# Kernel tuning notes

Hardware: AMD Instinct MI355X
Metric: run time of the kernel (lower is better)

Reference implementation:

```python
import jax, jax.numpy as jnp
import numpy as np

B, C, H, W = 4, 512, 64, 64
NUM_GROUPS = 32
EPS = 1e-6


def setup_inputs() -> dict:
    key = jax.random.key(0)
    ks = jax.random.split(key, 5)
    s = 1.0 / np.sqrt(C)
    return {
        "x": jax.random.normal(ks[0], (B, C, H, W), dtype=jnp.float32),
        "gn_scale": jnp.ones((C,), jnp.float32),
        "gn_bias": jnp.zeros((C,), jnp.float32),
        "wq": jax.random.normal(ks[1], (C, C), jnp.float32) * s,
        "bq": jnp.zeros((C,), jnp.float32),
        "wk": jax.random.normal(ks[2], (C, C), jnp.float32) * s,
        "bk": jnp.zeros((C,), jnp.float32),
        "wv": jax.random.normal(ks[3], (C, C), jnp.float32) * s,
        "bv": jnp.zeros((C,), jnp.float32),
        "wo": jax.random.normal(ks[4], (C, C), jnp.float32) * s,
        "bo": jnp.zeros((C,), jnp.float32),
    }


def _group_norm(x, scale, bias):
    # x: [b, c, h, w]; normalize over (c//g, h, w) within each of g groups
    b, c, h, w = x.shape
    g = NUM_GROUPS
    xg = x.reshape(b, g, c // g, h, w)
    mean = jnp.mean(xg, axis=(2, 3, 4), keepdims=True)
    var = jnp.var(xg, axis=(2, 3, 4), keepdims=True)
    xg = (xg - mean) * jax.lax.rsqrt(var + EPS)
    xn = xg.reshape(b, c, h, w)
    return xn * scale[None, :, None, None] + bias[None, :, None, None]


def _conv1x1(x, w, b):
    # channel-mixing 1x1 conv: [b, c, h, w] x [c_in, c_out] -> [b, c_out, h, w]
    return jnp.einsum('bchw,cd->bdhw', x, w) + b[None, :, None, None]


def reference(x, gn_scale, gn_bias, wq, bq, wk, bk, wv, bv, wo, bo):
    b, c, h, w = x.shape
    h_ = _group_norm(x, gn_scale, gn_bias)
    q = _conv1x1(h_, wq, bq).reshape(b, c, h * w).transpose(0, 2, 1)  # [b, hw, c]
    k = _conv1x1(h_, wk, bk).reshape(b, c, h * w)                     # [b, c, hw]
    v = _conv1x1(h_, wv, bv).reshape(b, c, h * w)                     # [b, c, hw]
    scores = jnp.matmul(q, k) * (c ** -0.5)      # [b, hw, hw]
    attn = jax.nn.softmax(scores, axis=-1)       # [b, hw, hw]
    out = jnp.matmul(v, attn.transpose(0, 2, 1)) # [b, c, hw]
    out = out.reshape(b, c, h, w)
    out = _conv1x1(out, wo, bo)
    return x + out
```

## Files before the change

### kernel.cpp

```cpp
#include <hip/hip_runtime.h>
#include <stdint.h>

typedef __attribute__((ext_vector_type(8))) short short8;
typedef __attribute__((ext_vector_type(4))) float f32x4;
typedef __attribute__((ext_vector_type(16))) float f32x16;
typedef __attribute__((ext_vector_type(4))) unsigned int uint4v;

__device__ __forceinline__ short cvt_bf16(float f) {
  uint32_t u = __builtin_bit_cast(uint32_t, f);
  u += 0x7FFFu + ((u >> 16) & 1u);
  return (short)(u >> 16);
}

__device__ __forceinline__ float bf16_to_f32(short s) {
  return __builtin_bit_cast(float, (uint32_t)((unsigned short)s) << 16);
}

__device__ __forceinline__ void gload_lds16(const void* g, void* l) {
  __builtin_amdgcn_global_load_lds(
      (const __attribute__((address_space(1))) void*)g,
      (__attribute__((address_space(3))) void*)l, 16, 0, 0);
}

__global__ __launch_bounds__(256) void k_transpose_w(const float* __restrict__ src,
                                                     short* __restrict__ dst) {
  __shared__ float t[32][33];
  int n0 = blockIdx.x * 32, c0 = blockIdx.y * 32;
  int lx = threadIdx.x & 31, ly = threadIdx.x >> 5;
#pragma unroll
  for (int i = 0; i < 4; ++i) {
    int c = ly + i * 8;
    t[c][lx] = src[(size_t)(c0 + c) * 512 + n0 + lx];
  }
  __syncthreads();
#pragma unroll
  for (int i = 0; i < 4; ++i) {
    int n = ly + i * 8;
    dst[(size_t)(n0 + n) * 512 + c0 + lx] = cvt_bf16(t[lx][n]);
  }
}

__global__ void k_bias_concat(const float* __restrict__ bq, const float* __restrict__ bk,
                              float* __restrict__ bqk) {
  int i = blockIdx.x * 256 + threadIdx.x;
  if (i < 512) bqk[i] = bq[i];
  else if (i < 1024) bqk[i] = bk[i - 512];
}

__global__ __launch_bounds__(256) void k_gn_stats(const float* __restrict__ x,
                                                  float* __restrict__ stats) {
  int bg = blockIdx.x;
  const float* p = x + (size_t)bg * 65536;
  float s = 0.f, ss = 0.f;
#pragma unroll 4
  for (int i = 0; i < 64; ++i) {
    float4 v = *(const float4*)(p + i * 1024 + threadIdx.x * 4);
    s += v.x + v.y + v.z + v.w;
    ss += v.x * v.x + v.y * v.y + v.z * v.z + v.w * v.w;
  }
#pragma unroll
  for (int m = 1; m < 64; m <<= 1) {
    s += __shfl_xor(s, m, 64);
    ss += __shfl_xor(ss, m, 64);
  }
  __shared__ float red[8];
  int w = threadIdx.x >> 6;
  if ((threadIdx.x & 63) == 0) { red[w * 2] = s; red[w * 2 + 1] = ss; }
  __syncthreads();
  if (threadIdx.x == 0) {
    float S1 = red[0] + red[2] + red[4] + red[6];
    float S2 = red[1] + red[3] + red[5] + red[7];
    float mean = S1 * (1.f / 65536.f);
    float var = S2 * (1.f / 65536.f) - mean * mean;
    stats[bg * 2] = mean;
    stats[bg * 2 + 1] = rsqrtf(var + 1e-6f);
  }
}

__global__ __launch_bounds__(256) void k_gn_apply(const float* __restrict__ x,
    const float* __restrict__ stats, const float* __restrict__ gsc,
    const float* __restrict__ gbi, short* __restrict__ h_t) {
  __shared__ float t[64][65];
  int p0 = blockIdx.x * 64, c0 = blockIdx.y * 64, b = blockIdx.z;
  int lp = threadIdx.x & 63, lc = threadIdx.x >> 6;
#pragma unroll
  for (int i = 0; i < 16; ++i) {
    int c = c0 + lc * 16 + i;
    float mean = stats[(b * 32 + (c >> 4)) * 2];
    float rstd = stats[(b * 32 + (c >> 4)) * 2 + 1];
    float v = x[((size_t)b * 512 + c) * 4096 + p0 + lp];
    t[lc * 16 + i][lp] = (v - mean) * rstd * gsc[c] + gbi[c];
  }
  __syncthreads();
  int pl = threadIdx.x >> 2;
  int cs = (threadIdx.x & 3) * 16;
  short8 v8a, v8b;
#pragma unroll
  for (int j = 0; j < 8; ++j) v8a[j] = cvt_bf16(t[cs + j][pl]);
#pragma unroll
  for (int j = 0; j < 8; ++j) v8b[j] = cvt_bf16(t[cs + 8 + j][pl]);
  size_t o = ((size_t)(b * 4096 + p0 + pl)) * 512 + c0 + cs;
  *(short8*)(h_t + o) = v8a;
  *(short8*)(h_t + o + 8) = v8b;
}

template <int BIAS_M, int FINAL>
__global__ __launch_bounds__(256) void k_gemm(const short* __restrict__ A,
    const short* __restrict__ Bm, const float* __restrict__ bias,
    short* __restrict__ Cb, float* __restrict__ Cf, const float* __restrict__ resid,
    int ldc) {
  __shared__ __align__(16) short a_lds[128 * 32];
  __shared__ __align__(16) short b_lds[128 * 32];
  int m0 = blockIdx.x * 128, n0 = blockIdx.y * 128;
  int lane = threadIdx.x & 63, wid = threadIdx.x >> 6;
  int h16 = lane >> 4, l16 = lane & 15;
  int wr = wid >> 1, wc = wid & 1;

  f32x4 acc[4][4];
#pragma unroll
  for (int mi = 0; mi < 4; ++mi)
#pragma unroll
    for (int ni = 0; ni < 4; ++ni) acc[mi][ni] = (f32x4){0.f, 0.f, 0.f, 0.f};

  for (int kk = 0; kk < 16; ++kk) {
#pragma unroll
    for (int i = 0; i < 4; ++i) {
      int idx = wid * 4 + i;
      int mat = idx >> 3, h = (idx >> 1) & 3, rh = idx & 1;
      const short* src = (mat ? Bm : A) +
          ((size_t)((mat ? n0 : m0) + rh * 64 + lane)) * 512 + kk * 32 + h * 8;
      short* dst = (mat ? b_lds : a_lds) + (h * 128 + rh * 64) * 8;
      gload_lds16(src, dst);
    }
    asm volatile("s_waitcnt vmcnt(0)" ::: "memory");
    __syncthreads();
    short8 af[4], bf[4];
#pragma unroll
    for (int mi = 0; mi < 4; ++mi)
      af[mi] = *(const short8*)(a_lds + (h16 * 128 + wr * 64 + mi * 16 + l16) * 8);
#pragma unroll
    for (int ni = 0; ni < 4; ++ni)
      bf[ni] = *(const short8*)(b_lds + (h16 * 128 + wc * 64 + ni * 16 + l16) * 8);
#pragma unroll
    for (int mi = 0; mi < 4; ++mi)
#pragma unroll
      for (int ni = 0; ni < 4; ++ni)
        acc[mi][ni] = __builtin_amdgcn_mfma_f32_16x16x32_bf16(af[mi], bf[ni], acc[mi][ni], 0, 0, 0);
    __syncthreads();
  }

#pragma unroll
  for (int mi = 0; mi < 4; ++mi)
#pragma unroll
    for (int ni = 0; ni < 4; ++ni)
#pragma unroll
      for (int r = 0; r < 4; ++r) {
        int row = m0 + wr * 64 + mi * 16 + 4 * h16 + r;
        int col = n0 + wc * 64 + ni * 16 + l16;
        float v = acc[mi][ni][r] + (BIAS_M ? bias[row] : bias[col]);
        if (FINAL) {
          size_t oidx = ((size_t)((col >> 12) * 512 + row)) * 4096 + (col & 4095);
          Cf[oidx] = v + resid[oidx];
        } else {
          Cb[(size_t)row * ldc + col] = cvt_bf16(v);
        }
      }
}

__global__ __launch_bounds__(512, 2) void k_flash6(const short* __restrict__ qk,
    const short* __restrict__ v_t, short* __restrict__ oa, short* __restrict__ ob,
    float* __restrict__ ml) {
  __shared__ __align__(16) short k_lds[2 * 32 * 512];
  __shared__ __align__(16) short v_lds[32 * 512];
  __shared__ __align__(16) float s_lds[8 * 1024];

  const int tid = threadIdx.x;
  const int lane = tid & 63, wid = tid >> 6;
  const int qg = wid >> 1, dh = wid & 1;
  const int l31 = lane & 31, h = lane >> 5;
  const int bx = blockIdx.x;
  const int combo = bx & 7, qt = bx >> 3;
  const int b = combo >> 1, s = combo & 1;
  const float K2 = 0.06376649f;

  short8 qf[16];
  {
    const short* qbase = qk + ((size_t)(b * 4096 + qt * 128 + qg * 32 + l31)) * 1024
                         + dh * 256 + h * 8;
#pragma unroll
    for (int s_ = 0; s_ < 16; ++s_) qf[s_] = *(const short8*)(qbase + s_ * 16);
  }

  const size_t kvrow0 = (size_t)(b * 4096 + s * 2048);

#define STAGE_K6(T, DST)                                                              \
  {                                                                                   \
    int t_ = (T);                                                                     \
    short* d_ = (DST);                                                                \
    _Pragma("unroll") for (int i = 0; i < 4; ++i) {                                   \
      int ks = wid * 4 + i;                                                           \
      gload_lds16(qk + (kvrow0 + t_ * 32 + l31) * 1024 + 512 + ks * 16 + h * 8,       \
                  d_ + ks * 512);                                                     \
    }                                                                                 \
  }
#define STAGE_V6(T)                                                                   \
  {                                                                                   \
    int t_ = (T);                                                                     \
    _Pragma("unroll") for (int i = 0; i < 4; ++i) {                                   \
      int si = wid * 4 + i;                                                           \
      int ks = si >> 4, d0 = si & 15;                                                 \
      gload_lds16(v_t + (size_t)(d0 * 32 + l31) * 16384                               \
                      + (kvrow0 + t_ * 32 + ks * 16 + h * 8),                         \
                  v_lds + si * 512);                                                  \
    }                                                                                 \
  }

  STAGE_K6(0, k_lds);
  STAGE_V6(0);
  asm volatile("s_waitcnt vmcnt(0)" ::: "memory");
  __builtin_amdgcn_s_barrier();
  __builtin_amdgcn_sched_barrier(0);

  float m_run = -3.0e38f, l_run = 0.f;
  f32x16 acc[8];
#pragma unroll
  for (int tl = 0; tl < 8; ++tl)
#pragma unroll
    for (int r = 0; r < 16; ++r) acc[tl][r] = 0.f;

  for (int t = 0; t < 64; ++t) {
    const int kb = t & 1;
    const short* kcur = k_lds + kb * (32 * 512);
    short* knxt = k_lds + (kb ^ 1) * (32 * 512);
    if (t + 1 < 64) STAGE_K6(t + 1, knxt);
    f32x16 st;
#pragma unroll
    for (int r = 0; r < 16; ++r) st[r] = 0.f;
    __builtin_amdgcn_s_setprio(1);
#pragma unroll
    for (int s_ = 0; s_ < 16; ++s_) {
      short8 kf = *(const short8*)(kcur + ((dh * 16 + s_) * 64 + lane) * 8);
      st = __builtin_amdgcn_mfma_f32_32x32x16_bf16(kf, qf[s_], st, 0, 0, 0);
    }
    __builtin_amdgcn_s_setprio(0);
    {
      float* sp = s_lds + wid * 1024 + lane * 4;
#pragma unroll
      for (int q4 = 0; q4 < 4; ++q4) {
        f32x4 v = {st[q4 * 4 + 0], st[q4 * 4 + 1], st[q4 * 4 + 2], st[q4 * 4 + 3]};
        *(f32x4*)(sp + q4 * 256) = v;
      }
    }
    asm volatile("s_waitcnt vmcnt(4) lgkmcnt(0)" ::: "memory");
    __builtin_amdgcn_s_barrier();
    __builtin_amdgcn_sched_barrier(0);
    {
      const float* sp = s_lds + (wid ^ 1) * 1024 + lane * 4;
#pragma unroll
      for (int q4 = 0; q4 < 4; ++q4) {
        f32x4 v = *(const f32x4*)(sp + q4 * 256);
        st[q4 * 4 + 0] += v[0]; st[q4 * 4 + 1] += v[1];
        st[q4 * 4 + 2] += v[2]; st[q4 * 4 + 3] += v[3];
      }
    }
    float u0 = fmaxf(st[0], st[1]),  u1 = fmaxf(st[2], st[3]);
    float u2 = fmaxf(st[4], st[5]),  u3 = fmaxf(st[6], st[7]);
    float u4 = fmaxf(st[8], st[9]),  u5 = fmaxf(st[10], st[11]);
    float u6 = fmaxf(st[12], st[13]), u7 = fmaxf(st[14], st[15]);
    float mt = fmaxf(fmaxf(fmaxf(u0, u1), fmaxf(u2, u3)),
                     fmaxf(fmaxf(u4, u5), fmaxf(u6, u7)));
    mt = fmaxf(mt, __shfl_xor(mt, 32));
    if (__any(mt > m_run + 45.0f)) {
      float mnew = fmaxf(m_run, mt);
      float rs = exp2f((m_run - mnew) * K2);
      m_run = mnew;
      l_run *= rs;
#pragma unroll
      for (int r = 0; r < 16; ++r) {
        int rowq = (r & 3) + 8 * (r >> 2) + 4 * h;
        float rr = __shfl(rs, rowq);
#pragma unroll
        for (int tl = 0; tl < 8; ++tl) acc[tl][r] *= rr;
      }
    }
    float ls = 0.f;
#pragma unroll
    for (int r = 0; r < 16; ++r) { st[r] = exp2f((st[r] - m_run) * K2); ls += st[r]; }
    ls += __shfl_xor(ls, 32);
    l_run += ls;
    __builtin_amdgcn_s_setprio(1);
#pragma unroll
    for (int ks = 0; ks < 2; ++ks) {
      unsigned int a0, a1, a2, a3;
      int bse = ks * 8;
      asm("v_cvt_pk_bf16_f32 %0, %1, %2" : "=v"(a0) : "v"(st[bse + 0]), "v"(st[bse + 1]));
      asm("v_cvt_pk_bf16_f32 %0, %1, %2" : "=v"(a1) : "v"(st[bse + 2]), "v"(st[bse + 3]));
      asm("v_cvt_pk_bf16_f32 %0, %1, %2" : "=v"(a2) : "v"(st[bse + 4]), "v"(st[bse + 5]));
      asm("v_cvt_pk_bf16_f32 %0, %1, %2" : "=v"(a3) : "v"(st[bse + 6]), "v"(st[bse + 7]));
      asm("v_permlane32_swap_b32 %0, %1" : "+v"(a0), "+v"(a2));
      asm("v_permlane32_swap_b32 %0, %1" : "+v"(a1), "+v"(a3));
      uint4v w; w[0] = a0; w[1] = a1; w[2] = a2; w[3] = a3;
      short8 pa = __builtin_bit_cast(short8, w);
#pragma unroll
      for (int tl = 0; tl < 8; ++tl) {
        short8 vb = *(const short8*)(v_lds + ((ks * 16 + dh * 8 + tl) * 64 + lane) * 8);
        acc[tl] = __builtin_amdgcn_mfma_f32_32x32x16_bf16(pa, vb, acc[tl], 0, 0, 0);
      }
    }
    __builtin_amdgcn_s_setprio(0);
    asm volatile("s_waitcnt vmcnt(0) lgkmcnt(0)" ::: "memory");
    __builtin_amdgcn_s_barrier();
    __builtin_amdgcn_sched_barrier(0);
    if (t + 1 < 64) STAGE_V6(t + 1);
  }

  float linv = 1.0f / l_run;
  short* obuf = (s == 0) ? oa : ob;
#pragma unroll
  for (int r = 0; r < 16; ++r) {
    int rowq = (r & 3) + 8 * (r >> 2) + 4 * h;
    float li = __shfl(linv, rowq);
    size_t grow = ((size_t)(b * 4096 + qt * 128 + qg * 32 + rowq)) * 512;
#pragma unroll
    for (int tl = 0; tl < 8; ++tl)
      obuf[grow + dh * 256 + tl * 32 + l31] = cvt_bf16(acc[tl][r] * li);
  }
  if (dh == 0 && lane < 32) {
    int gq = b * 4096 + qt * 128 + qg * 32 + lane;
    ml[((size_t)s * 16384 + gq) * 2 + 0] = m_run;
    ml[((size_t)s * 16384 + gq) * 2 + 1] = l_run;
  }
#undef STAGE_K6
#undef STAGE_V6
}

__global__ __launch_bounds__(256) void k_combine(const short* __restrict__ oa,
    const float* __restrict__ ml, short* __restrict__ ob_out) {
  int gq = blockIdx.x * 4 + (threadIdx.x >> 6);
  int d0 = (threadIdx.x & 63) * 8;
  const float K2 = 0.06376649f;
  float ma = ml[(size_t)gq * 2 + 0], la = ml[(size_t)gq * 2 + 1];
  float mb = ml[((size_t)16384 + gq) * 2 + 0], lb = ml[((size_t)16384 + gq) * 2 + 1];
  float m = fmaxf(ma, mb);
  float wa = exp2f((ma - m) * K2) * la;
  float wb = exp2f((mb - m) * K2) * lb;
  float denom = wa + wb;
  float fa, fb;
  if (isfinite(denom) && denom > 0.f) {
    float inv = 1.f / denom;
    fa = wa * inv; fb = wb * inv;
  } else {
    fa = (ma >= mb) ? 1.f : 0.f;
    fb = 1.f - fa;
  }
  short8 a = *(const short8*)(oa + (size_t)gq * 512 + d0);
  short8 bv = *(const short8*)(ob_out + (size_t)gq * 512 + d0);
  short8 o;
#pragma unroll
  for (int j = 0; j < 8; ++j)
    o[j] = cvt_bf16(fa * bf16_to_f32(a[j]) + fb * bf16_to_f32(bv[j]));
  *(short8*)(ob_out + (size_t)gq * 512 + d0) = o;
}

extern "C" void kernel_launch(void* const* d_in, const int* in_sizes, int n_in,
                              void* d_out, int out_size, void* d_ws, size_t ws_size,
                              hipStream_t stream) {
  const float* x   = (const float*)d_in[0];
  const float* gsc = (const float*)d_in[1];
  const float* gbi = (const float*)d_in[2];
  const float* wq  = (const float*)d_in[3];
  const float* bq  = (const float*)d_in[4];
  const float* wk  = (const float*)d_in[5];
  const float* bk  = (const float*)d_in[6];
  const float* wv  = (const float*)d_in[7];
  const float* bv  = (const float*)d_in[8];
  const float* wo  = (const float*)d_in[9];
  const float* bo  = (const float*)d_in[10];
  float* out = (float*)d_out;

  char* ws = (char*)d_ws;
  float* stats = (float*)ws;
  float* bqk   = (float*)(ws + 4096);
  short* wqk_t = (short*)(ws + 16384);
  short* wv_t  = (short*)(ws + 16384 + (1u << 20));
  short* wo_t  = (short*)(ws + 16384 + (1u << 20) + (1u << 19));
  char*  big   = ws + 16384 + (1u << 21);
  short* h_t   = (short*)big;
  short* qkb   = (short*)(big + (16ll << 20));
  short* v_t   = (short*)(big + (48ll << 20));
  short* o_at  = (short*)(big + (64ll << 20));
  float* mlbuf = (float*)(big + (80ll << 20));

  dim3 b256(256);
  k_transpose_w<<<dim3(16, 16), b256, 0, stream>>>(wq, wqk_t);
  k_transpose_w<<<dim3(16, 16), b256, 0, stream>>>(wk, wqk_t + 512 * 512);
  k_transpose_w<<<dim3(16, 16), b256, 0, stream>>>(wv, wv_t);
  k_transpose_w<<<dim3(16, 16), b256, 0, stream>>>(wo, wo_t);
  k_bias_concat<<<4, 256, 0, stream>>>(bq, bk, bqk);
  k_gn_stats<<<128, b256, 0, stream>>>(x, stats);
  k_gn_apply<<<dim3(64, 8, 4), b256, 0, stream>>>(x, stats, gsc, gbi, h_t);
  k_gemm<0, 0><<<dim3(128, 8), b256, 0, stream>>>(h_t, wqk_t, bqk, qkb, nullptr, nullptr, 1024);
  k_gemm<1, 0><<<dim3(4, 128), b256, 0, stream>>>(wv_t, h_t, bv, v_t, nullptr, nullptr, 16384);
  k_flash6<<<dim3(256), dim3(512), 0, stream>>>(qkb, v_t, h_t, o_at, mlbuf);
  k_combine<<<dim3(4096), b256, 0, stream>>>(h_t, mlbuf, o_at);
  k_gemm<1, 1><<<dim3(4, 128), b256, 0, stream>>>(wo_t, o_at, bo, nullptr, out, x, 0);
}
```

Measured before the change: 401.7 us.

## Shrink flash attention blocks to 64 queries, single-buffer K, split QK accumulator chains

```diff
diff --git a/kernel.cpp b/kernel.cpp
--- a/kernel.cpp
+++ b/kernel.cpp
@@ -167,12 +167,12 @@
       }
 }
 
-__global__ __launch_bounds__(512, 2) void k_flash6(const short* __restrict__ qk,
+__global__ __launch_bounds__(256, 2) void k_flash7(const short* __restrict__ qk,
     const short* __restrict__ v_t, short* __restrict__ oa, short* __restrict__ ob,
     float* __restrict__ ml) {
-  __shared__ __align__(16) short k_lds[2 * 32 * 512];
+  __shared__ __align__(16) short k_lds[32 * 512];
   __shared__ __align__(16) short v_lds[32 * 512];
-  __shared__ __align__(16) float s_lds[8 * 1024];
+  __shared__ __align__(16) float s_lds[4 * 1024];
 
   const int tid = threadIdx.x;
   const int lane = tid & 63, wid = tid >> 6;
@@ -185,7 +185,7 @@
 
   short8 qf[16];
   {
-    const short* qbase = qk + ((size_t)(b * 4096 + qt * 128 + qg * 32 + l31)) * 1024
+    const short* qbase = qk + ((size_t)(b * 4096 + qt * 64 + qg * 32 + l31)) * 1024
                          + dh * 256 + h * 8;
 #pragma unroll
     for (int s_ = 0; s_ < 16; ++s_) qf[s_] = *(const short8*)(qbase + s_ * 16);
@@ -193,21 +193,20 @@
 
   const size_t kvrow0 = (size_t)(b * 4096 + s * 2048);
 
-#define STAGE_K6(T, DST)                                                              \
+#define STAGE_K7(T)                                                                   \
   {                                                                                   \
     int t_ = (T);                                                                     \
-    short* d_ = (DST);                                                                \
-    _Pragma("unroll") for (int i = 0; i < 4; ++i) {                                   \
-      int ks = wid * 4 + i;                                                           \
+    _Pragma("unroll") for (int i = 0; i < 8; ++i) {                                   \
+      int ks = wid * 8 + i;                                                           \
       gload_lds16(qk + (kvrow0 + t_ * 32 + l31) * 1024 + 512 + ks * 16 + h * 8,       \
-                  d_ + ks * 512);                                                     \
+                  k_lds + ks * 512);                                                  \
     }                                                                                 \
   }
-#define STAGE_V6(T)                                                                   \
+#define STAGE_V7(T)                                                                   \
   {                                                                                   \
     int t_ = (T);                                                                     \
-    _Pragma("unroll") for (int i = 0; i < 4; ++i) {                                   \
-      int si = wid * 4 + i;                                                           \
+    _Pragma("unroll") for (int i = 0; i < 8; ++i) {                                   \
+      int si = wid * 8 + i;                                                           \
       int ks = si >> 4, d0 = si & 15;                                                 \
       gload_lds16(v_t + (size_t)(d0 * 32 + l31) * 16384                               \
                       + (kvrow0 + t_ * 32 + ks * 16 + h * 8),                         \
@@ -215,8 +214,8 @@
     }                                                                                 \
   }
 
-  STAGE_K6(0, k_lds);
-  STAGE_V6(0);
+  STAGE_K7(0);
+  STAGE_V7(0);
   asm volatile("s_waitcnt vmcnt(0)" ::: "memory");
   __builtin_amdgcn_s_barrier();
   __builtin_amdgcn_sched_barrier(0);
@@ -229,20 +228,22 @@
     for (int r = 0; r < 16; ++r) acc[tl][r] = 0.f;
 
   for (int t = 0; t < 64; ++t) {
-    const int kb = t & 1;
-    const short* kcur = k_lds + kb * (32 * 512);
-    short* knxt = k_lds + (kb ^ 1) * (32 * 512);
-    if (t + 1 < 64) STAGE_K6(t + 1, knxt);
+    const int tn = (t + 1 < 64) ? t + 1 : 63;
+    f32x16 stA, stB;
+#pragma unroll
+    for (int r = 0; r < 16; ++r) { stA[r] = 0.f; stB[r] = 0.f; }
+    __builtin_amdgcn_s_setprio(1);
+#pragma unroll
+    for (int s_ = 0; s_ < 8; ++s_) {
+      short8 kfA = *(const short8*)(k_lds + ((dh * 16 + s_) * 64 + lane) * 8);
+      short8 kfB = *(const short8*)(k_lds + ((dh * 16 + 8 + s_) * 64 + lane) * 8);
+      stA = __builtin_amdgcn_mfma_f32_32x32x16_bf16(kfA, qf[s_], stA, 0, 0, 0);
+      stB = __builtin_amdgcn_mfma_f32_32x32x16_bf16(kfB, qf[8 + s_], stB, 0, 0, 0);
+    }
+    __builtin_amdgcn_s_setprio(0);
     f32x16 st;
 #pragma unroll
-    for (int r = 0; r < 16; ++r) st[r] = 0.f;
-    __builtin_amdgcn_s_setprio(1);
-#pragma unroll
-    for (int s_ = 0; s_ < 16; ++s_) {
-      short8 kf = *(const short8*)(kcur + ((dh * 16 + s_) * 64 + lane) * 8);
-      st = __builtin_amdgcn_mfma_f32_32x32x16_bf16(kf, qf[s_], st, 0, 0, 0);
-    }
-    __builtin_amdgcn_s_setprio(0);
+    for (int r = 0; r < 16; ++r) st[r] = stA[r] + stB[r];
     {
       float* sp = s_lds + wid * 1024 + lane * 4;
 #pragma unroll
@@ -251,9 +252,10 @@
         *(f32x4*)(sp + q4 * 256) = v;
       }
     }
-    asm volatile("s_waitcnt vmcnt(4) lgkmcnt(0)" ::: "memory");
+    asm volatile("s_waitcnt vmcnt(0) lgkmcnt(0)" ::: "memory");
     __builtin_amdgcn_s_barrier();
     __builtin_amdgcn_sched_barrier(0);
+    STAGE_K7(tn);
     {
       const float* sp = s_lds + (wid ^ 1) * 1024 + lane * 4;
 #pragma unroll
@@ -311,7 +313,7 @@
     asm volatile("s_waitcnt vmcnt(0) lgkmcnt(0)" ::: "memory");
     __builtin_amdgcn_s_barrier();
     __builtin_amdgcn_sched_barrier(0);
-    if (t + 1 < 64) STAGE_V6(t + 1);
+    STAGE_V7(tn);
   }
 
   float linv = 1.0f / l_run;
@@ -320,18 +322,18 @@
   for (int r = 0; r < 16; ++r) {
     int rowq = (r & 3) + 8 * (r >> 2) + 4 * h;
     float li = __shfl(linv, rowq);
-    size_t grow = ((size_t)(b * 4096 + qt * 128 + qg * 32 + rowq)) * 512;
+    size_t grow = ((size_t)(b * 4096 + qt * 64 + qg * 32 + rowq)) * 512;
 #pragma unroll
     for (int tl = 0; tl < 8; ++tl)
       obuf[grow + dh * 256 + tl * 32 + l31] = cvt_bf16(acc[tl][r] * li);
   }
   if (dh == 0 && lane < 32) {
-    int gq = b * 4096 + qt * 128 + qg * 32 + lane;
+    int gq = b * 4096 + qt * 64 + qg * 32 + lane;
     ml[((size_t)s * 16384 + gq) * 2 + 0] = m_run;
     ml[((size_t)s * 16384 + gq) * 2 + 1] = l_run;
   }
-#undef STAGE_K6
-#undef STAGE_V6
+#undef STAGE_K7
+#undef STAGE_V7
 }
 
 __global__ __launch_bounds__(256) void k_combine(const short* __restrict__ oa,
@@ -401,7 +403,7 @@
   k_gn_apply<<<dim3(64, 8, 4), b256, 0, stream>>>(x, stats, gsc, gbi, h_t);
   k_gemm<0, 0><<<dim3(128, 8), b256, 0, stream>>>(h_t, wqk_t, bqk, qkb, nullptr, nullptr, 1024);
   k_gemm<1, 0><<<dim3(4, 128), b256, 0, stream>>>(wv_t, h_t, bv, v_t, nullptr, nullptr, 16384);
-  k_flash6<<<dim3(256), dim3(512), 0, stream>>>(qkb, v_t, h_t, o_at, mlbuf);
+  k_flash7<<<dim3(512), b256, 0, stream>>>(qkb, v_t, h_t, o_at, mlbuf);
   k_combine<<<dim3(4096), b256, 0, stream>>>(h_t, mlbuf, o_at);
   k_gemm<1, 1><<<dim3(4, 128), b256, 0, stream>>>(wo_t, o_at, bo, nullptr, out, x, 0);
 }
```

New measurement: 548.8 us. +36.6%, slower.

## Software-pipeline flash attention: overlap QK of next tile with softmax/PV of previous

Applied to the files above, without the earlier changes.

```diff
diff --git a/kernel.cpp b/kernel.cpp
--- a/kernel.cpp
+++ b/kernel.cpp
@@ -167,11 +167,11 @@
       }
 }
 
-__global__ __launch_bounds__(512, 2) void k_flash6(const short* __restrict__ qk,
+__global__ __launch_bounds__(512, 2) void k_flash8(const short* __restrict__ qk,
     const short* __restrict__ v_t, short* __restrict__ oa, short* __restrict__ ob,
     float* __restrict__ ml) {
-  __shared__ __align__(16) short k_lds[2 * 32 * 512];
-  __shared__ __align__(16) short v_lds[32 * 512];
+  __shared__ __align__(16) short k_lds[32 * 512];
+  __shared__ __align__(16) short v_lds[2 * 32 * 512];
   __shared__ __align__(16) float s_lds[8 * 1024];
 
   const int tid = threadIdx.x;
@@ -193,125 +193,159 @@
 
   const size_t kvrow0 = (size_t)(b * 4096 + s * 2048);
 
-#define STAGE_K6(T, DST)                                                              \
+#define STAGE_K8(T)                                                                   \
+  {                                                                                   \
+    int t_ = (T);                                                                     \
+    _Pragma("unroll") for (int i = 0; i < 4; ++i) {                                   \
+      int ks = wid * 4 + i;                                                           \
+      gload_lds16(qk + (kvrow0 + t_ * 32 + l31) * 1024 + 512 + ks * 16 + h * 8,       \
+                  k_lds + ks * 512);                                                  \
+    }                                                                                 \
+  }
+#define STAGE_V8(T, DST)                                                              \
   {                                                                                   \
     int t_ = (T);                                                                     \
     short* d_ = (DST);                                                                \
-    _Pragma("unroll") for (int i = 0; i < 4; ++i) {                                   \
-      int ks = wid * 4 + i;                                                           \
-      gload_lds16(qk + (kvrow0 + t_ * 32 + l31) * 1024 + 512 + ks * 16 + h * 8,       \
-                  d_ + ks * 512);                                                     \
-    }                                                                                 \
-  }
-#define STAGE_V6(T)                                                                   \
-  {                                                                                   \
-    int t_ = (T);                                                                     \
     _Pragma("unroll") for (int i = 0; i < 4; ++i) {                                   \
       int si = wid * 4 + i;                                                           \
       int ks = si >> 4, d0 = si & 15;                                                 \
       gload_lds16(v_t + (size_t)(d0 * 32 + l31) * 16384                               \
                       + (kvrow0 + t_ * 32 + ks * 16 + h * 8),                         \
-                  v_lds + si * 512);                                                  \
-    }                                                                                 \
-  }
-
-  STAGE_K6(0, k_lds);
-  STAGE_V6(0);
+                  d_ + si * 512);                                                     \
+    }                                                                                 \
+  }
+#define QK8(ST)                                                                       \
+  _Pragma("unroll") for (int s_ = 0; s_ < 16; ++s_) {                                 \
+    short8 kf = *(const short8*)(k_lds + ((dh * 16 + s_) * 64 + lane) * 8);           \
+    ST = __builtin_amdgcn_mfma_f32_32x32x16_bf16(kf, qf[s_], ST, 0, 0, 0);            \
+  }
+#define SOFTMAX8(STC, PA)                                                             \
+  {                                                                                   \
+    float u0 = fmaxf(STC[0], STC[1]),  u1 = fmaxf(STC[2], STC[3]);                    \
+    float u2 = fmaxf(STC[4], STC[5]),  u3 = fmaxf(STC[6], STC[7]);                    \
+    float u4 = fmaxf(STC[8], STC[9]),  u5 = fmaxf(STC[10], STC[11]);                  \
+    float u6 = fmaxf(STC[12], STC[13]), u7 = fmaxf(STC[14], STC[15]);                 \
+    float mt = fmaxf(fmaxf(fmaxf(u0, u1), fmaxf(u2, u3)),                             \
+                     fmaxf(fmaxf(u4, u5), fmaxf(u6, u7)));                            \
+    mt = fmaxf(mt, __shfl_xor(mt, 32));                                               \
+    if (__any(mt > m_run + 45.0f)) {                                                  \
+      float mnew = fmaxf(m_run, mt);                                                  \
+      float rs = exp2f((m_run - mnew) * K2);                                          \
+      m_run = mnew;                                                                   \
+      l_run *= rs;                                                                    \
+      _Pragma("unroll") for (int r = 0; r < 16; ++r) {                                \
+        int rowq = (r & 3) + 8 * (r >> 2) + 4 * h;                                    \
+        float rr = __shfl(rs, rowq);                                                  \
+        _Pragma("unroll") for (int tl = 0; tl < 8; ++tl) acc[tl][r] *= rr;            \
+      }                                                                               \
+    }                                                                                 \
+    float ls = 0.f;                                                                   \
+    _Pragma("unroll") for (int r = 0; r < 16; ++r) {                                  \
+      STC[r] = exp2f((STC[r] - m_run) * K2); ls += STC[r];                            \
+    }                                                                                 \
+    ls += __shfl_xor(ls, 32);                                                         \
+    l_run += ls;                                                                      \
+    _Pragma("unroll") for (int ks = 0; ks < 2; ++ks) {                                \
+      unsigned int a0, a1, a2, a3;                                                    \
+      int bse = ks * 8;                                                               \
+      asm("v_cvt_pk_bf16_f32 %0, %1, %2" : "=v"(a0) : "v"(STC[bse+0]), "v"(STC[bse+1])); \
+      asm("v_cvt_pk_bf16_f32 %0, %1, %2" : "=v"(a1) : "v"(STC[bse+2]), "v"(STC[bse+3])); \
+      asm("v_cvt_pk_bf16_f32 %0, %1, %2" : "=v"(a2) : "v"(STC[bse+4]), "v"(STC[bse+5])); \
+      asm("v_cvt_pk_bf16_f32 %0, %1, %2" : "=v"(a3) : "v"(STC[bse+6]), "v"(STC[bse+7])); \
+      asm("v_permlane32_swap_b32 %0, %1" : "+v"(a0), "+v"(a2));                       \
+      asm("v_permlane32_swap_b32 %0, %1" : "+v"(a1), "+v"(a3));                       \
+      uint4v w; w[0] = a0; w[1] = a1; w[2] = a2; w[3] = a3;                           \
+      PA[ks] = __builtin_bit_cast(short8, w);                                         \
+    }                                                                                 \
+  }
+#define SWRITE8(ST)                                                                   \
+  {                                                                                   \
+    float* sp = s_lds + wid * 1024 + lane * 4;                                        \
+    _Pragma("unroll") for (int q4 = 0; q4 < 4; ++q4) {                                \
+      f32x4 v = {ST[q4*4+0], ST[q4*4+1], ST[q4*4+2], ST[q4*4+3]};                     \
+      *(f32x4*)(sp + q4 * 256) = v;                                                   \
+    }                                                                                 \
+  }
+#define SCOMBINE8(ST, STC)                                                            \
+  {                                                                                   \
+    const float* sp = s_lds + (wid ^ 1) * 1024 + lane * 4;                            \
+    _Pragma("unroll") for (int q4 = 0; q4 < 4; ++q4) {                                \
+      f32x4 v = *(const f32x4*)(sp + q4 * 256);                                       \
+      STC[q4*4+0] = ST[q4*4+0] + v[0]; STC[q4*4+1] = ST[q4*4+1] + v[1];               \
+      STC[q4*4+2] = ST[q4*4+2] + v[2]; STC[q4*4+3] = ST[q4*4+3] + v[3];               \
+    }                                                                                 \
+  }
+#define PV8(PA, VSRC)                                                                 \
+  _Pragma("unroll") for (int ks = 0; ks < 2; ++ks)                                    \
+    _Pragma("unroll") for (int tl = 0; tl < 8; ++tl) {                                \
+      short8 vb = *(const short8*)((VSRC) + ((ks * 16 + dh * 8 + tl) * 64 + lane) * 8); \
+      acc[tl] = __builtin_amdgcn_mfma_f32_32x32x16_bf16(PA[ks], vb, acc[tl], 0, 0, 0); \
+    }
+
+  float m_run = -3.0e38f, l_run = 0.f;
+  f32x16 acc[8];
+#pragma unroll
+  for (int tl = 0; tl < 8; ++tl)
+#pragma unroll
+    for (int r = 0; r < 16; ++r) acc[tl][r] = 0.f;
+
+  STAGE_K8(0);
+  STAGE_V8(0, v_lds);
   asm volatile("s_waitcnt vmcnt(0)" ::: "memory");
   __builtin_amdgcn_s_barrier();
   __builtin_amdgcn_sched_barrier(0);
 
-  float m_run = -3.0e38f, l_run = 0.f;
-  f32x16 acc[8];
-#pragma unroll
-  for (int tl = 0; tl < 8; ++tl)
-#pragma unroll
-    for (int r = 0; r < 16; ++r) acc[tl][r] = 0.f;
-
-  for (int t = 0; t < 64; ++t) {
-    const int kb = t & 1;
-    const short* kcur = k_lds + kb * (32 * 512);
-    short* knxt = k_lds + (kb ^ 1) * (32 * 512);
-    if (t + 1 < 64) STAGE_K6(t + 1, knxt);
+  f32x16 stC;
+  {
     f32x16 st;
 #pragma unroll
     for (int r = 0; r < 16; ++r) st[r] = 0.f;
     __builtin_amdgcn_s_setprio(1);
-#pragma unroll
-    for (int s_ = 0; s_ < 16; ++s_) {
-      short8 kf = *(const short8*)(kcur + ((dh * 16 + s_) * 64 + lane) * 8);
-      st = __builtin_amdgcn_mfma_f32_32x32x16_bf16(kf, qf[s_], st, 0, 0, 0);
-    }
+    QK8(st);
     __builtin_amdgcn_s_setprio(0);
-    {
-      float* sp = s_lds + wid * 1024 + lane * 4;
-#pragma unroll
-      for (int q4 = 0; q4 < 4; ++q4) {
-        f32x4 v = {st[q4 * 4 + 0], st[q4 * 4 + 1], st[q4 * 4 + 2], st[q4 * 4 + 3]};
-        *(f32x4*)(sp + q4 * 256) = v;
-      }
-    }
-    asm volatile("s_waitcnt vmcnt(4) lgkmcnt(0)" ::: "memory");
+    SWRITE8(st);
+    asm volatile("s_waitcnt lgkmcnt(0)" ::: "memory");
     __builtin_amdgcn_s_barrier();
     __builtin_amdgcn_sched_barrier(0);
-    {
-      const float* sp = s_lds + (wid ^ 1) * 1024 + lane * 4;
-#pragma unroll
-      for (int q4 = 0; q4 < 4; ++q4) {
-        f32x4 v = *(const f32x4*)(sp + q4 * 256);
-        st[q4 * 4 + 0] += v[0]; st[q4 * 4 + 1] += v[1];
-        st[q4 * 4 + 2] += v[2]; st[q4 * 4 + 3] += v[3];
-      }
-    }
-    float u0 = fmaxf(st[0], st[1]),  u1 = fmaxf(st[2], st[3]);
-    float u2 = fmaxf(st[4], st[5]),  u3 = fmaxf(st[6], st[7]);
-    float u4 = fmaxf(st[8], st[9]),  u5 = fmaxf(st[10], st[11]);
-    float u6 = fmaxf(st[12], st[13]), u7 = fmaxf(st[14], st[15]);
-    float mt = fmaxf(fmaxf(fmaxf(u0, u1), fmaxf(u2, u3)),
-                     fmaxf(fmaxf(u4, u5), fmaxf(u6, u7)));
-    mt = fmaxf(mt, __shfl_xor(mt, 32));
-    if (__any(mt > m_run + 45.0f)) {
-      float mnew = fmaxf(m_run, mt);
-      float rs = exp2f((m_run - mnew) * K2);
-      m_run = mnew;
-      l_run *= rs;
-#pragma unroll
-      for (int r = 0; r < 16; ++r) {
-        int rowq = (r & 3) + 8 * (r >> 2) + 4 * h;
-        float rr = __shfl(rs, rowq);
-#pragma unroll
-        for (int tl = 0; tl < 8; ++tl) acc[tl][r] *= rr;
-      }
-    }
-    float ls = 0.f;
-#pragma unroll
-    for (int r = 0; r < 16; ++r) { st[r] = exp2f((st[r] - m_run) * K2); ls += st[r]; }
-    ls += __shfl_xor(ls, 32);
-    l_run += ls;
+    STAGE_K8(1);
+    SCOMBINE8(st, stC);
+    asm volatile("s_waitcnt vmcnt(0) lgkmcnt(0)" ::: "memory");
+    __builtin_amdgcn_s_barrier();
+    __builtin_amdgcn_sched_barrier(0);
+    STAGE_V8(1, v_lds + 32 * 512);
+  }
+
+  for (int t = 1; t < 64; ++t) {
+    const int tn = (t + 1 < 64) ? t + 1 : 63;
+    const short* vprev = v_lds + ((t - 1) & 1) * (32 * 512);
+    short* vnext = v_lds + ((t + 1) & 1) * (32 * 512);
+    f32x16 st;
+#pragma unroll
+    for (int r = 0; r < 16; ++r) st[r] = 0.f;
     __builtin_amdgcn_s_setprio(1);
-#pragma unroll
-    for (int ks = 0; ks < 2; ++ks) {
-      unsigned int a0, a1, a2, a3;
-      int bse = ks * 8;
-      asm("v_cvt_pk_bf16_f32 %0, %1, %2" : "=v"(a0) : "v"(st[bse + 0]), "v"(st[bse + 1]));
-      asm("v_cvt_pk_bf16_f32 %0, %1, %2" : "=v"(a1) : "v"(st[bse + 2]), "v"(st[bse + 3]));
-      asm("v_cvt_pk_bf16_f32 %0, %1, %2" : "=v"(a2) : "v"(st[bse + 4]), "v"(st[bse + 5]));
-      asm("v_cvt_pk_bf16_f32 %0, %1, %2" : "=v"(a3) : "v"(st[bse + 6]), "v"(st[bse + 7]));
-      asm("v_permlane32_swap_b32 %0, %1" : "+v"(a0), "+v"(a2));
-      asm("v_permlane32_swap_b32 %0, %1" : "+v"(a1), "+v"(a3));
-      uint4v w; w[0] = a0; w[1] = a1; w[2] = a2; w[3] = a3;
-      short8 pa = __builtin_bit_cast(short8, w);
-#pragma unroll
-      for (int tl = 0; tl < 8; ++tl) {
-        short8 vb = *(const short8*)(v_lds + ((ks * 16 + dh * 8 + tl) * 64 + lane) * 8);
-        acc[tl] = __builtin_amdgcn_mfma_f32_32x32x16_bf16(pa, vb, acc[tl], 0, 0, 0);
-      }
-    }
+    QK8(st);
+    __builtin_amdgcn_s_setprio(0);
+    short8 pa[2];
+    SOFTMAX8(stC, pa);
+    SWRITE8(st);
+    asm volatile("s_waitcnt lgkmcnt(0)" ::: "memory");
+    __builtin_amdgcn_s_barrier();
+    __builtin_amdgcn_sched_barrier(0);
+    if (t < 63) STAGE_K8(tn);
+    SCOMBINE8(st, stC);
+    __builtin_amdgcn_s_setprio(1);
+    PV8(pa, vprev);
     __builtin_amdgcn_s_setprio(0);
     asm volatile("s_waitcnt vmcnt(0) lgkmcnt(0)" ::: "memory");
     __builtin_amdgcn_s_barrier();
     __builtin_amdgcn_sched_barrier(0);
-    if (t + 1 < 64) STAGE_V6(t + 1);
+    if (t < 63) STAGE_V8(tn, vnext);
+  }
+
+  {
+    short8 pa[2];
+    SOFTMAX8(stC, pa);
+    PV8(pa, v_lds + (63 & 1) * (32 * 512));
   }
 
   float linv = 1.0f / l_run;
@@ -330,8 +364,13 @@
     ml[((size_t)s * 16384 + gq) * 2 + 0] = m_run;
     ml[((size_t)s * 16384 + gq) * 2 + 1] = l_run;
   }
-#undef STAGE_K6
-#undef STAGE_V6
+#undef STAGE_K8
+#undef STAGE_V8
+#undef QK8
+#undef SOFTMAX8
+#undef SWRITE8
+#undef SCOMBINE8
+#undef PV8
 }
 
 __global__ __launch_bounds__(256) void k_combine(const short* __restrict__ oa,
@@ -401,7 +440,7 @@
   k_gn_apply<<<dim3(64, 8, 4), b256, 0, stream>>>(x, stats, gsc, gbi, h_t);
   k_gemm<0, 0><<<dim3(128, 8), b256, 0, stream>>>(h_t, wqk_t, bqk, qkb, nullptr, nullptr, 1024);
   k_gemm<1, 0><<<dim3(4, 128), b256, 0, stream>>>(wv_t, h_t, bv, v_t, nullptr, nullptr, 16384);
-  k_flash6<<<dim3(256), dim3(512), 0, stream>>>(qkb, v_t, h_t, o_at, mlbuf);
+  k_flash8<<<dim3(256), dim3(512), 0, stream>>>(qkb, v_t, h_t, o_at, mlbuf);
   k_combine<<<dim3(4096), b256, 0, stream>>>(h_t, mlbuf, o_at);
   k_gemm<1, 1><<<dim3(4, 128), b256, 0, stream>>>(wo_t, o_at, bo, nullptr, out, x, 0);
 }
```

After: 379.2 us. 5.6% less time.

## Process 64-key tiles per flash iteration with bf16 partial-score exchange

Applied to the files above, without the earlier changes.

```diff
diff --git a/kernel.cpp b/kernel.cpp
--- a/kernel.cpp
+++ b/kernel.cpp
@@ -14,6 +14,13 @@
 
 __device__ __forceinline__ float bf16_to_f32(short s) {
   return __builtin_bit_cast(float, (uint32_t)((unsigned short)s) << 16);
+}
+
+__device__ __forceinline__ float bflo(uint32_t u) {
+  return __builtin_bit_cast(float, u << 16);
+}
+__device__ __forceinline__ float bfhi(uint32_t u) {
+  return __builtin_bit_cast(float, u & 0xffff0000u);
 }
 
 __device__ __forceinline__ void gload_lds16(const void* g, void* l) {
@@ -167,12 +174,12 @@
       }
 }
 
-__global__ __launch_bounds__(512, 2) void k_flash6(const short* __restrict__ qk,
+__global__ __launch_bounds__(512, 2) void k_flash9(const short* __restrict__ qk,
     const short* __restrict__ v_t, short* __restrict__ oa, short* __restrict__ ob,
     float* __restrict__ ml) {
-  __shared__ __align__(16) short k_lds[2 * 32 * 512];
-  __shared__ __align__(16) short v_lds[32 * 512];
-  __shared__ __align__(16) float s_lds[8 * 1024];
+  __shared__ __align__(16) short k_lds[64 * 512];
+  __shared__ __align__(16) short v_lds[64 * 512];
+  __shared__ __align__(16) char  s_x[8 * 4096];
 
   const int tid = threadIdx.x;
   const int lane = tid & 63, wid = tid >> 6;
@@ -193,30 +200,31 @@
 
   const size_t kvrow0 = (size_t)(b * 4096 + s * 2048);
 
-#define STAGE_K6(T, DST)                                                              \
+#define STAGE_K9(T)                                                                   \
   {                                                                                   \
     int t_ = (T);                                                                     \
-    short* d_ = (DST);                                                                \
-    _Pragma("unroll") for (int i = 0; i < 4; ++i) {                                   \
-      int ks = wid * 4 + i;                                                           \
-      gload_lds16(qk + (kvrow0 + t_ * 32 + l31) * 1024 + 512 + ks * 16 + h * 8,       \
-                  d_ + ks * 512);                                                     \
+    _Pragma("unroll") for (int i = 0; i < 8; ++i) {                                   \
+      int idx = wid * 8 + i;                                                          \
+      int u = idx >> 5, ks = idx & 31;                                                \
+      gload_lds16(qk + (kvrow0 + t_ * 64 + u * 32 + l31) * 1024 + 512 + ks * 16 + h * 8, \
+                  k_lds + idx * 512);                                                 \
     }                                                                                 \
   }
-#define STAGE_V6(T)                                                                   \
+#define STAGE_V9(T)                                                                   \
   {                                                                                   \
     int t_ = (T);                                                                     \
-    _Pragma("unroll") for (int i = 0; i < 4; ++i) {                                   \
-      int si = wid * 4 + i;                                                           \
+    _Pragma("unroll") for (int i = 0; i < 8; ++i) {                                   \
+      int idx = wid * 8 + i;                                                          \
+      int u = idx >> 5, si = idx & 31;                                                \
       int ks = si >> 4, d0 = si & 15;                                                 \
       gload_lds16(v_t + (size_t)(d0 * 32 + l31) * 16384                               \
-                      + (kvrow0 + t_ * 32 + ks * 16 + h * 8),                         \
-                  v_lds + si * 512);                                                  \
+                      + (kvrow0 + t_ * 64 + u * 32 + ks * 16 + h * 8),                \
+                  v_lds + idx * 512);                                                 \
     }                                                                                 \
   }
 
-  STAGE_K6(0, k_lds);
-  STAGE_V6(0);
+  STAGE_K9(0);
+  STAGE_V9(0);
   asm volatile("s_waitcnt vmcnt(0)" ::: "memory");
   __builtin_amdgcn_s_barrier();
   __builtin_amdgcn_sched_barrier(0);
@@ -228,90 +236,113 @@
 #pragma unroll
     for (int r = 0; r < 16; ++r) acc[tl][r] = 0.f;
 
-  for (int t = 0; t < 64; ++t) {
-    const int kb = t & 1;
-    const short* kcur = k_lds + kb * (32 * 512);
-    short* knxt = k_lds + (kb ^ 1) * (32 * 512);
-    if (t + 1 < 64) STAGE_K6(t + 1, knxt);
-    f32x16 st;
-#pragma unroll
-    for (int r = 0; r < 16; ++r) st[r] = 0.f;
+  for (int t = 0; t < 32; ++t) {
+    f32x16 st0, st1;
+#pragma unroll
+    for (int r = 0; r < 16; ++r) { st0[r] = 0.f; st1[r] = 0.f; }
     __builtin_amdgcn_s_setprio(1);
 #pragma unroll
     for (int s_ = 0; s_ < 16; ++s_) {
-      short8 kf = *(const short8*)(kcur + ((dh * 16 + s_) * 64 + lane) * 8);
-      st = __builtin_amdgcn_mfma_f32_32x32x16_bf16(kf, qf[s_], st, 0, 0, 0);
+      short8 kf0 = *(const short8*)(k_lds + ((dh * 16 + s_) * 64 + lane) * 8);
+      short8 kf1 = *(const short8*)(k_lds + ((32 + dh * 16 + s_) * 64 + lane) * 8);
+      st0 = __builtin_amdgcn_mfma_f32_32x32x16_bf16(kf0, qf[s_], st0, 0, 0, 0);
+      st1 = __builtin_amdgcn_mfma_f32_32x32x16_bf16(kf1, qf[s_], st1, 0, 0, 0);
     }
     __builtin_amdgcn_s_setprio(0);
     {
-      float* sp = s_lds + wid * 1024 + lane * 4;
-#pragma unroll
-      for (int q4 = 0; q4 < 4; ++q4) {
-        f32x4 v = {st[q4 * 4 + 0], st[q4 * 4 + 1], st[q4 * 4 + 2], st[q4 * 4 + 3]};
-        *(f32x4*)(sp + q4 * 256) = v;
+      uint32_t pk[16];
+#pragma unroll
+      for (int g = 0; g < 8; ++g)
+        asm("v_cvt_pk_bf16_f32 %0, %1, %2" : "=v"(pk[g]) : "v"(st0[2 * g]), "v"(st0[2 * g + 1]));
+#pragma unroll
+      for (int g = 0; g < 8; ++g)
+        asm("v_cvt_pk_bf16_f32 %0, %1, %2" : "=v"(pk[8 + g]) : "v"(st1[2 * g]), "v"(st1[2 * g + 1]));
+      char* smine = s_x + wid * 4096 + lane * 16;
+#pragma unroll
+      for (int g = 0; g < 4; ++g) {
+        uint4v w; w[0] = pk[4 * g]; w[1] = pk[4 * g + 1]; w[2] = pk[4 * g + 2]; w[3] = pk[4 * g + 3];
+        *(uint4v*)(smine + g * 1024) = w;
       }
     }
-    asm volatile("s_waitcnt vmcnt(4) lgkmcnt(0)" ::: "memory");
+    asm volatile("s_waitcnt vmcnt(0) lgkmcnt(0)" ::: "memory");
     __builtin_amdgcn_s_barrier();
     __builtin_amdgcn_sched_barrier(0);
+    if (t + 1 < 32) STAGE_K9(t + 1);
     {
-      const float* sp = s_lds + (wid ^ 1) * 1024 + lane * 4;
-#pragma unroll
-      for (int q4 = 0; q4 < 4; ++q4) {
-        f32x4 v = *(const f32x4*)(sp + q4 * 256);
-        st[q4 * 4 + 0] += v[0]; st[q4 * 4 + 1] += v[1];
-        st[q4 * 4 + 2] += v[2]; st[q4 * 4 + 3] += v[3];
+      const char* sp = s_x + (wid ^ 1) * 4096 + lane * 16;
+#pragma unroll
+      for (int g = 0; g < 4; ++g) {
+        uint4v p = *(const uint4v*)(sp + g * 1024);
+#pragma unroll
+        for (int c = 0; c < 4; ++c) {
+          int k = g * 4 + c;
+          float lo = bflo(p[c]), hi = bfhi(p[c]);
+          if (k < 8) { st0[2 * k] += lo; st0[2 * k + 1] += hi; }
+          else       { st1[2 * (k - 8)] += lo; st1[2 * (k - 8) + 1] += hi; }
+        }
       }
     }
-    float u0 = fmaxf(st[0], st[1]),  u1 = fmaxf(st[2], st[3]);
-    float u2 = fmaxf(st[4], st[5]),  u3 = fmaxf(st[6], st[7]);
-    float u4 = fmaxf(st[8], st[9]),  u5 = fmaxf(st[10], st[11]);
-    float u6 = fmaxf(st[12], st[13]), u7 = fmaxf(st[14], st[15]);
-    float mt = fmaxf(fmaxf(fmaxf(u0, u1), fmaxf(u2, u3)),
-                     fmaxf(fmaxf(u4, u5), fmaxf(u6, u7)));
-    mt = fmaxf(mt, __shfl_xor(mt, 32));
-    if (__any(mt > m_run + 45.0f)) {
-      float mnew = fmaxf(m_run, mt);
-      float rs = exp2f((m_run - mnew) * K2);
-      m_run = mnew;
-      l_run *= rs;
-#pragma unroll
-      for (int r = 0; r < 16; ++r) {
-        int rowq = (r & 3) + 8 * (r >> 2) + 4 * h;
-        float rr = __shfl(rs, rowq);
-#pragma unroll
-        for (int tl = 0; tl < 8; ++tl) acc[tl][r] *= rr;
+    {
+      float u0 = fmaxf(fmaxf(st0[0], st0[1]), fmaxf(st0[2], st0[3]));
+      float u1 = fmaxf(fmaxf(st0[4], st0[5]), fmaxf(st0[6], st0[7]));
+      float u2 = fmaxf(fmaxf(st0[8], st0[9]), fmaxf(st0[10], st0[11]));
+      float u3 = fmaxf(fmaxf(st0[12], st0[13]), fmaxf(st0[14], st0[15]));
+      float u4 = fmaxf(fmaxf(st1[0], st1[1]), fmaxf(st1[2], st1[3]));
+      float u5 = fmaxf(fmaxf(st1[4], st1[5]), fmaxf(st1[6], st1[7]));
+      float u6 = fmaxf(fmaxf(st1[8], st1[9]), fmaxf(st1[10], st1[11]));
+      float u7 = fmaxf(fmaxf(st1[12], st1[13]), fmaxf(st1[14], st1[15]));
+      float mt = fmaxf(fmaxf(fmaxf(u0, u1), fmaxf(u2, u3)),
+                       fmaxf(fmaxf(u4, u5), fmaxf(u6, u7)));
+      mt = fmaxf(mt, __shfl_xor(mt, 32));
+      if (__any(mt > m_run + 45.0f)) {
+        float mnew = fmaxf(m_run, mt);
+        float rs = exp2f((m_run - mnew) * K2);
+        m_run = mnew;
+        l_run *= rs;
+#pragma unroll
+        for (int r = 0; r < 16; ++r) {
+          int rowq = (r & 3) + 8 * (r >> 2) + 4 * h;
+          float rr = __shfl(rs, rowq);
+#pragma unroll
+          for (int tl = 0; tl < 8; ++tl) acc[tl][r] *= rr;
+        }
       }
-    }
-    float ls = 0.f;
-#pragma unroll
-    for (int r = 0; r < 16; ++r) { st[r] = exp2f((st[r] - m_run) * K2); ls += st[r]; }
-    ls += __shfl_xor(ls, 32);
-    l_run += ls;
+      float ls = 0.f;
+#pragma unroll
+      for (int r = 0; r < 16; ++r) { st0[r] = exp2f((st0[r] - m_run) * K2); ls += st0[r]; }
+#pragma unroll
+      for (int r = 0; r < 16; ++r) { st1[r] = exp2f((st1[r] - m_run) * K2); ls += st1[r]; }
+      ls += __shfl_xor(ls, 32);
+      l_run += ls;
+    }
     __builtin_amdgcn_s_setprio(1);
 #pragma unroll
-    for (int ks = 0; ks < 2; ++ks) {
-      unsigned int a0, a1, a2, a3;
-      int bse = ks * 8;
-      asm("v_cvt_pk_bf16_f32 %0, %1, %2" : "=v"(a0) : "v"(st[bse + 0]), "v"(st[bse + 1]));
-      asm("v_cvt_pk_bf16_f32 %0, %1, %2" : "=v"(a1) : "v"(st[bse + 2]), "v"(st[bse + 3]));
-      asm("v_cvt_pk_bf16_f32 %0, %1, %2" : "=v"(a2) : "v"(st[bse + 4]), "v"(st[bse + 5]));
-      asm("v_cvt_pk_bf16_f32 %0, %1, %2" : "=v"(a3) : "v"(st[bse + 6]), "v"(st[bse + 7]));
-      asm("v_permlane32_swap_b32 %0, %1" : "+v"(a0), "+v"(a2));
-      asm("v_permlane32_swap_b32 %0, %1" : "+v"(a1), "+v"(a3));
-      uint4v w; w[0] = a0; w[1] = a1; w[2] = a2; w[3] = a3;
-      short8 pa = __builtin_bit_cast(short8, w);
-#pragma unroll
-      for (int tl = 0; tl < 8; ++tl) {
-        short8 vb = *(const short8*)(v_lds + ((ks * 16 + dh * 8 + tl) * 64 + lane) * 8);
-        acc[tl] = __builtin_amdgcn_mfma_f32_32x32x16_bf16(pa, vb, acc[tl], 0, 0, 0);
+    for (int u = 0; u < 2; ++u) {
+#pragma unroll
+      for (int ks = 0; ks < 2; ++ks) {
+        unsigned int a0, a1, a2, a3;
+        int bse = ks * 8;
+        const f32x16& stu = u ? st1 : st0;
+        asm("v_cvt_pk_bf16_f32 %0, %1, %2" : "=v"(a0) : "v"(stu[bse + 0]), "v"(stu[bse + 1]));
+        asm("v_cvt_pk_bf16_f32 %0, %1, %2" : "=v"(a1) : "v"(stu[bse + 2]), "v"(stu[bse + 3]));
+        asm("v_cvt_pk_bf16_f32 %0, %1, %2" : "=v"(a2) : "v"(stu[bse + 4]), "v"(stu[bse + 5]));
+        asm("v_cvt_pk_bf16_f32 %0, %1, %2" : "=v"(a3) : "v"(stu[bse + 6]), "v"(stu[bse + 7]));
+        asm("v_permlane32_swap_b32 %0, %1" : "+v"(a0), "+v"(a2));
+        asm("v_permlane32_swap_b32 %0, %1" : "+v"(a1), "+v"(a3));
+        uint4v w; w[0] = a0; w[1] = a1; w[2] = a2; w[3] = a3;
+        short8 pa = __builtin_bit_cast(short8, w);
+#pragma unroll
+        for (int tl = 0; tl < 8; ++tl) {
+          short8 vb = *(const short8*)(v_lds + ((u * 32 + ks * 16 + dh * 8 + tl) * 64 + lane) * 8);
+          acc[tl] = __builtin_amdgcn_mfma_f32_32x32x16_bf16(pa, vb, acc[tl], 0, 0, 0);
+        }
       }
     }
     __builtin_amdgcn_s_setprio(0);
     asm volatile("s_waitcnt vmcnt(0) lgkmcnt(0)" ::: "memory");
     __builtin_amdgcn_s_barrier();
     __builtin_amdgcn_sched_barrier(0);
-    if (t + 1 < 64) STAGE_V6(t + 1);
+    if (t + 1 < 32) STAGE_V9(t + 1);
   }
 
   float linv = 1.0f / l_run;
@@ -330,8 +361,8 @@
     ml[((size_t)s * 16384 + gq) * 2 + 0] = m_run;
     ml[((size_t)s * 16384 + gq) * 2 + 1] = l_run;
   }
-#undef STAGE_K6
-#undef STAGE_V6
+#undef STAGE_K9
+#undef STAGE_V9
 }
 
 __global__ __launch_bounds__(256) void k_combine(const short* __restrict__ oa,
@@ -401,7 +432,7 @@
   k_gn_apply<<<dim3(64, 8, 4), b256, 0, stream>>>(x, stats, gsc, gbi, h_t);
   k_gemm<0, 0><<<dim3(128, 8), b256, 0, stream>>>(h_t, wqk_t, bqk, qkb, nullptr, nullptr, 1024);
   k_gemm<1, 0><<<dim3(4, 128), b256, 0, stream>>>(wv_t, h_t, bv, v_t, nullptr, nullptr, 16384);
-  k_flash6<<<dim3(256), dim3(512), 0, stream>>>(qkb, v_t, h_t, o_at, mlbuf);
+  k_flash9<<<dim3(256), dim3(512), 0, stream>>>(qkb, v_t, h_t, o_at, mlbuf);
   k_combine<<<dim3(4096), b256, 0, stream>>>(h_t, mlbuf, o_at);
   k_gemm<1, 1><<<dim3(4, 128), b256, 0, stream>>>(wo_t, o_at, bo, nullptr, out, x, 0);
 }
```

Measured after the change: 743.6 us. 1.85x slower.
